# Kernel optimization log

Measured on AMD Instinct MI355X. Metric: run time of the kernel, lower is better.

Reference implementation:

```python
import jax, jax.numpy as jnp
from jax import lax
import numpy as np

B, H, W, C = 4, 64, 64, 128
L = H * W
DI = 2 * C   # mamba d_inner (expand=2)
NS = 16      # d_state
R = C // 16  # dt_rank
K = 4        # d_conv
S = 4        # scan branches: fwd, bwd, extra1, extra2


def setup_inputs():
    key = jax.random.key(0)
    ks = jax.random.split(key, 20)
    g = lambda i, shape, s=0.02: jax.random.normal(ks[i], shape, jnp.float32) * s
    return {
        "I1": jax.random.normal(ks[0], (B, L, C), jnp.float32),
        "fusion_resi": jax.random.normal(ks[1], (B, L, C), jnp.float32),
        "I2": jax.random.normal(ks[2], (B, L, C), jnp.float32),
        "fusion": jax.random.normal(ks[3], (B, L, C), jnp.float32),
        "ln1_w": jnp.ones((C,)), "ln1_b": jnp.zeros((C,)),
        "ln2_w": jnp.ones((C,)), "ln2_b": jnp.zeros((C,)),
        "ln3_w": jnp.ones((C,)), "ln3_b": jnp.zeros((C,)),
        "sp_w": g(4, (1, 2, 5, 5), 0.1),
        "ca_w1": g(5, (C // 4, C), 0.05),
        "ca_w2": g(6, (C, C // 4), 0.05),
        "dw_w": g(7, (C, 1, 3, 3), 0.1),
        "dw_b": jnp.zeros((C,)),
        "in_proj_w": g(8, (2 * DI, C)),
        "in_proj1_w": g(9, (DI, C)),
        "in_proj2_w": g(10, (DI, C)),
        "conv_w": g(11, (S, DI, K), 0.1),
        "conv_b": jnp.zeros((S, DI)),
        "xproj_w": g(12, (S, R + 2 * NS, DI)),
        "dt_w": g(13, (S, DI, R), 0.1),
        "dt_b": jnp.full((S, DI), -4.6, jnp.float32),  # softplus -> dt ~ 0.01
        "A_log": jnp.broadcast_to(jnp.log(jnp.arange(1, NS + 1, dtype=jnp.float32)), (S, DI, NS)) * 1.0,
        "Dskip": jnp.ones((S, DI)),
        "out_w": g(14, (C, DI)),
        "test_h": H, "test_w": W,
    }


def ln(x, w, b):
    mu = x.mean(-1, keepdims=True)
    xc = x - mu
    v = (xc * xc).mean(-1, keepdims=True)
    return xc / jnp.sqrt(v + 1e-5) * w + b


def sp_att(x, w, h, wd):
    # x: (B, N, C) -> (B, N, 1) spatial attention map
    Bb = x.shape[0]
    m = jnp.concatenate([x.mean(2, keepdims=True), x.max(2, keepdims=True)], 2)
    m = m.transpose(0, 2, 1).reshape(Bb, 2, h, wd)
    o = lax.conv_general_dilated(m, w, (1, 1), [(2, 2), (2, 2)],
                                 dimension_numbers=("NCHW", "OIHW", "NCHW"))
    return jax.nn.sigmoid(o).reshape(Bb, 1, -1).transpose(0, 2, 1)


def mamba_m3(xf, e1, e2, in_proj_w, in_proj1_w, in_proj2_w, conv_w, conv_b,
             xproj_w, dt_w, dt_b, A_log, Dskip, out_w):
    Bb, Ll, _ = xf.shape
    xz = xf @ in_proj_w.T                       # (B,L,2DI)
    x, z = xz[..., :DI], xz[..., DI:]
    # 4 branches: forward, backward (flipped), extra_emb1, extra_emb2
    u = jnp.stack([x, x[:, ::-1], e1 @ in_proj1_w.T, e2 @ in_proj2_w.T], 0)  # (S,B,L,DI)

    def causal_dwconv(xb, w, b):                # xb (B,L,DI)
        xp = jnp.pad(xb.transpose(0, 2, 1), ((0, 0), (0, 0), (K - 1, 0)))
        o = lax.conv_general_dilated(xp, w[:, None, :], (1,), "VALID",
                                     feature_group_count=DI,
                                     dimension_numbers=("NCH", "OIH", "NCH"))
        return (o + b[None, :, None]).transpose(0, 2, 1)

    uc = jax.nn.silu(jax.vmap(causal_dwconv)(u, conv_w, conv_b))        # (S,B,L,DI)
    proj = jnp.einsum("sbld,spd->sblp", uc, xproj_w)
    dt = jax.nn.softplus(jnp.einsum("sblr,sdr->sbld", proj[..., :R], dt_w)
                         + dt_b[:, None, None, :])                      # (S,B,L,DI)
    Bm, Cm = proj[..., R:R + NS], proj[..., R + NS:]                    # (S,B,L,NS)
    A = -jnp.exp(A_log)                                                 # (S,DI,NS)

    def step(h, inp):
        dt_t, B_t, C_t, u_t = inp                                       # (S,B,DI),(S,B,NS),(S,B,NS),(S,B,DI)
        dA = jnp.exp(dt_t[..., None] * A[:, None])                      # (S,B,DI,NS)
        h = h * dA + (dt_t * u_t)[..., None] * B_t[:, :, None, :]
        return h, jnp.einsum("sbdn,sbn->sbd", h, C_t)

    xs = tuple(t.transpose(2, 0, 1, 3) for t in (dt, Bm, Cm, uc))
    h0 = jnp.zeros((S, Bb, DI, NS), xf.dtype)
    _, ys = lax.scan(step, h0, xs)                                      # (L,S,B,DI)
    y = ys.transpose(1, 2, 0, 3) + uc * Dskip[:, None, None, :]         # (S,B,L,DI)
    y_tot = y[0] + y[1][:, ::-1] + y[2] + y[3]
    return (y_tot * jax.nn.silu(z)) @ out_w.T


def reference(I1, fusion_resi, I2, fusion, ln1_w, ln1_b, ln2_w, ln2_b, ln3_w,
              ln3_b, sp_w, ca_w1, ca_w2, dw_w, dw_b, in_proj_w, in_proj1_w,
              in_proj2_w, conv_w, conv_b, xproj_w, dt_w, dt_b, A_log, Dskip,
              out_w, test_h, test_w):
    fusion_resi = fusion + fusion_resi
    fusion = ln(fusion_resi, ln1_w, ln1_b)
    I2 = ln(I2 * sp_att(I2, sp_w, test_h, test_w), ln2_w, ln2_b)
    I1 = ln(I1 * sp_att(I1, sp_w, test_h, test_w), ln3_w, ln3_b)
    # note: original applies norm1/norm2/norm3 a second time here (faithful)
    gf = mamba_m3(ln(fusion, ln1_w, ln1_b), ln(I2, ln2_w, ln2_b),
                  ln(I1, ln3_w, ln3_b), in_proj_w, in_proj1_w, in_proj2_w,
                  conv_w, conv_b, xproj_w, dt_w, dt_b, A_log, Dskip, out_w)
    Bb, _, Cc = gf.shape
    f4 = gf.transpose(0, 2, 1).reshape(Bb, Cc, test_h, test_w)
    # ChannelAttention1 (already returns x*sig) then extra *fusion per source
    fc = lambda v: jnp.maximum(v @ ca_w1.T, 0.0) @ ca_w2.T
    sig = jax.nn.sigmoid(fc(f4.mean((2, 3))) + fc(f4.max((2, 3))))[:, :, None, None]
    f4 = (f4 * sig) * f4
    dw = lax.conv_general_dilated(f4, dw_w, (1, 1), [(1, 1), (1, 1)],
                                  feature_group_count=Cc,
                                  dimension_numbers=("NCHW", "OIHW", "NCHW"))
    dw = dw + dw_b[None, :, None, None]
    out = (dw + f4).reshape(Bb, Cc, -1).transpose(0, 2, 1)
    return out, fusion_resi
```

## Files before the change

kernel.cpp:

```cpp
#include <hip/hip_runtime.h>

#define DEVI __device__ __forceinline__

static constexpr int BB=4, CC=128, LLn=4096, DI=256, NS=16, RR=8, SS=4;
static constexpr int PP = RR + 2*NS;
static constexpr int CT = 64, NCH = LLn/CT;
static constexpr size_t BLC  = (size_t)BB*LLn*CC;
static constexpr size_t BLD  = (size_t)BB*LLn*DI;
static constexpr size_t SBLD = (size_t)SS*BLD;
static constexpr size_t SBLP = (size_t)SS*BB*LLn*PP;

static constexpr int OW_LN1W=0, OW_LN1B=128, OW_LN2W=256, OW_LN2B=384, OW_LN3W=512, OW_LN3B=640,
 OW_SPW=768, OW_CAW1=820, OW_CAW2=4916, OW_DWW=9012, OW_DWB=10164, OW_IPW=10292,
 OW_IP1W=75828, OW_IP2W=108596, OW_CVW=141364, OW_CVB=145460, OW_XPW=146484,
 OW_DTW=187444, OW_DTB=195636, OW_ALOG=196660, OW_DSK=213044, OW_OUTW=214068;
static constexpr int NW_RAW = 246836;
static constexpr int NW_END = 246848;

__constant__ int c_woff[22] = {OW_LN1W,OW_LN1B,OW_LN2W,OW_LN2B,OW_LN3W,OW_LN3B,OW_SPW,OW_CAW1,
 OW_CAW2,OW_DWW,OW_DWB,OW_IPW,OW_IP1W,OW_IP2W,OW_CVW,OW_CVB,OW_XPW,OW_DTW,OW_DTB,OW_ALOG,
 OW_DSK,OW_OUTW};
__constant__ int c_wsz[22]  = {128,128,128,128,128,128,50,4096,4096,1152,128,65536,32768,32768,
 4096,1024,40960,8192,1024,16384,1024,32768};

static constexpr size_t O_XF   = NW_END;
static constexpr size_t O_E1   = O_XF + BLC;
static constexpr size_t O_E2   = O_E1 + BLC;
static constexpr size_t O_Z    = O_E2 + BLC;
static constexpr size_t O_U    = O_Z + BLD;
static constexpr size_t O_UC   = O_U + SBLD;
static constexpr size_t O_PROJ = O_UC + SBLD;
static constexpr size_t O_SDT  = O_PROJ + SBLP;
static constexpr size_t O_H    = O_SDT + (size_t)SS*BB*NCH*DI;
static constexpr size_t O_M    = O_H + (size_t)SS*BB*NCH*DI*NS;
static constexpr size_t O_S    = O_M + 2*(size_t)BB*2*LLn;
static constexpr size_t O_GF   = O_S + 2*(size_t)BB*LLn;
static constexpr size_t O_PART = O_GF + BLC;
static constexpr size_t O_SIG  = O_PART + 2*(size_t)BB*32*CC;
static constexpr size_t WS_END = O_SIG + (size_t)BB*CC;

typedef __attribute__((ext_vector_type(8))) short short8v;
typedef __attribute__((ext_vector_type(4))) float f32x4;

DEVI float bfu2f(unsigned short s){ union{unsigned u; float f;} c; c.u = ((unsigned)s)<<16; return c.f; }
DEVI unsigned short f2bfu(float f){ union{float f; unsigned u;} c; c.f=f;
  unsigned r = c.u + 0x7FFFu + ((c.u>>16)&1u); return (unsigned short)(r>>16); }
DEVI bool bfmode(const void* ln1w){ return *(const unsigned*)ln1w == 0x3F803F80u; }
DEVI float2 ldin2(const void* p, int i, bool isbf){
  if(isbf){ unsigned v = *(const unsigned*)((const unsigned short*)p + i);
    return make_float2(bfu2f((unsigned short)(v & 0xFFFFu)), bfu2f((unsigned short)(v >> 16))); }
  const float* f = (const float*)p + i; return make_float2(f[0], f[1]);
}
DEVI float wsum(float v){
#pragma unroll
  for(int o=32;o;o>>=1) v += __shfl_xor(v,o,64);
  return v; }
DEVI float wmaxr(float v){
#pragma unroll
  for(int o=32;o;o>>=1) v = fmaxf(v, __shfl_xor(v,o,64));
  return v; }
DEVI float sigf(float x){ return 1.f/(1.f+__expf(-x)); }
DEVI float2 ln_wave(float2 x, const float* Wf, int ow, int ob, int lane){
  float mu = wsum(x.x + x.y) * (1.f/(float)CC);
  float dx = x.x - mu, dy = x.y - mu;
  float var = wsum(dx*dx + dy*dy) * (1.f/(float)CC);
  float rs = rsqrtf(var + 1e-5f);
  int c = 2*lane;
  return make_float2(dx*rs*Wf[ow+c] + Wf[ob+c], dy*rs*Wf[ow+c+1] + Wf[ob+c+1]);
}

struct Srcs { const void* p[22]; };

__global__ void k_wcvt(Srcs s, float* __restrict__ ws,
                       unsigned short* __restrict__ wip, unsigned short* __restrict__ wob){
  bool isbf = bfmode(s.p[0]);
  int idx = blockIdx.x*256 + threadIdx.x;
  if(idx >= NW_RAW) return;
  int t = 0;
  while(t < 21 && idx >= c_woff[t+1]) t++;
  int j = idx - c_woff[t];
  if(j >= c_wsz[t]) return;
  float v = isbf ? bfu2f(((const unsigned short*)s.p[t])[j]) : ((const float*)s.p[t])[j];
  ws[idx] = v;
  if(t==11)      wip[j]         = f2bfu(v);
  else if(t==12) wip[65536+j]   = f2bfu(v);
  else if(t==13) wip[98304+j]   = f2bfu(v);
  else if(t==21) wob[j]         = f2bfu(v);
}

__global__ void k_fuse(const void* fus, const void* fres, const void* ln1raw,
                       float* __restrict__ ws, float* __restrict__ outf,
                       unsigned short* __restrict__ xbf){
  bool isbf = bfmode(ln1raw);
  int lane = threadIdx.x & 63, wv = threadIdx.x >> 6;
  int row = blockIdx.x*4 + wv;
  int base = row*CC;
  float2 a = ldin2(fus, base+2*lane, isbf);
  float2 b = ldin2(fres, base+2*lane, isbf);
  float2 fr = make_float2(a.x+b.x, a.y+b.y);
  *(float2*)(outf + BLC + base + 2*lane) = fr;
  float2 y = ln_wave(fr, ws, OW_LN1W, OW_LN1B, lane);
  y = ln_wave(y, ws, OW_LN1W, OW_LN1B, lane);
  unsigned pk = (unsigned)f2bfu(y.x) | ((unsigned)f2bfu(y.y)<<16);
  *(unsigned*)&xbf[base + 2*lane] = pk;
}

__global__ void k_meanmax(const void* I1, const void* I2, const void* ln1raw, float* __restrict__ ws){
  bool isbf = bfmode(ln1raw);
  int lane = threadIdx.x & 63, wv = threadIdx.x >> 6;
  int g = blockIdx.x*4 + wv;
  int ten = g & 1, row = g >> 1;
  const void* src = ten ? I2 : I1;
  float2 x = ldin2(src, row*CC + 2*lane, isbf);
  float sm = wsum(x.x + x.y) * (1.f/(float)CC);
  float mx = wmaxr(fmaxf(x.x, x.y));
  if(lane == 0){
    int b = row >> 12, l = row & 4095;
    float* mt = ws + O_M + (size_t)ten*(BB*2*LLn);
    mt[(size_t)b*2*LLn + l] = sm;
    mt[(size_t)b*2*LLn + LLn + l] = mx;
  }
}

__global__ void k_spconv(float* __restrict__ ws){
  int idx = blockIdx.x*256 + threadIdx.x;
  int ten = idx >> 14, b = (idx>>12)&3, l = idx & 4095;
  int h = l >> 6, w = l & 63;
  const float* mt = ws + O_M + (size_t)ten*(BB*2*LLn) + (size_t)b*2*LLn;
  float acc = 0.f;
  for(int ci=0; ci<2; ci++)
    for(int kh=0; kh<5; kh++){
      int hh = h + kh - 2; if((unsigned)hh >= 64u) continue;
      for(int kw=0; kw<5; kw++){
        int wn = w + kw - 2; if((unsigned)wn >= 64u) continue;
        acc += mt[(size_t)ci*LLn + hh*64 + wn] * ws[OW_SPW + ci*25 + kh*5 + kw];
      }
    }
  ws[O_S + (size_t)ten*(BB*LLn) + (size_t)b*LLn + l] = sigf(acc);
}

__global__ void k_escale(const void* I1, const void* I2, const void* ln1raw,
                         float* __restrict__ ws, unsigned short* __restrict__ xbf){
  bool isbf = bfmode(ln1raw);
  int lane = threadIdx.x & 63, wv = threadIdx.x >> 6;
  int g = blockIdx.x*4 + wv;
  int ten = g & 1, row = g >> 1;
  const void* src = ten ? I1 : I2;
  float sc = ws[O_S + (ten ? 0 : (size_t)BB*LLn) + row];
  float2 x = ldin2(src, row*CC + 2*lane, isbf);
  x.x *= sc; x.y *= sc;
  int ow = ten ? OW_LN3W : OW_LN2W, ob = ten ? OW_LN3B : OW_LN2B;
  float2 y = ln_wave(x, ws, ow, ob, lane);
  y = ln_wave(y, ws, ow, ob, lane);
  unsigned short* eb = xbf + (ten ? 2*BLC : BLC);
  unsigned pk = (unsigned)f2bfu(y.x) | ((unsigned)f2bfu(y.y)<<16);
  *(unsigned*)&eb[row*CC + 2*lane] = pk;
}

__global__ __launch_bounds__(256) void k_gemm_bf(const unsigned short* __restrict__ Abf,
    const unsigned short* __restrict__ Wbf, float* __restrict__ out,
    int Kd, int N, int mode, float* __restrict__ u, float* __restrict__ z){
  __shared__ unsigned short As[64*64];
  __shared__ unsigned short Bs[64*64];
  const int tid = threadIdx.x, lane = tid & 63, w = tid >> 6;
  const int n0 = blockIdx.x*64, m0 = blockIdx.y*64;
  const int g = lane >> 4, rlo = lane & 15;
  f32x4 acc[4];
#pragma unroll
  for(int i=0;i<4;i++) acc[i] = (f32x4){0.f,0.f,0.f,0.f};
  const int nk = Kd >> 6;
  for(int kt=0; kt<nk; kt++){
#pragma unroll
    for(int it=0; it<2; it++){
      int idx = it*256 + tid, r = idx>>3, c = idx&7;
      uint4 av = *(const uint4*)&Abf[(size_t)(m0+r)*Kd + kt*64 + c*8];
      uint4 bv = *(const uint4*)&Wbf[(size_t)(n0+r)*Kd + kt*64 + c*8];
      int sw = (c*16) ^ ((r&7)<<4);
      *(uint4*)((char*)As + r*128 + sw) = av;
      *(uint4*)((char*)Bs + r*128 + sw) = bv;
    }
    __syncthreads();
#pragma unroll
    for(int ks=0; ks<2; ks++){
      int kb = ks*64 + g*16;
      int brow = w*16 + rlo;
      short8v bf = *(short8v*)((char*)Bs + brow*128 + (kb ^ ((rlo&7)<<4)));
#pragma unroll
      for(int rt=0; rt<4; rt++){
        int arow = rt*16 + rlo;
        short8v af = *(short8v*)((char*)As + arow*128 + (kb ^ ((rlo&7)<<4)));
        acc[rt] = __builtin_amdgcn_mfma_f32_16x16x32_bf16(af, bf, acc[rt], 0, 0, 0);
      }
    }
    __syncthreads();
  }
#pragma unroll
  for(int rt=0; rt<4; rt++){
#pragma unroll
    for(int j=0; j<4; j++){
      int m = m0 + rt*16 + g*4 + j;
      int n = n0 + w*16 + rlo;
      float val = acc[rt][j];
      if(mode == 0){
        out[(size_t)m*N + n] = val;
      } else {
        int b = m >> 12, l = m & (LLn-1);
        if(n < DI){
          u[((size_t)b*LLn + l)*DI + n] = val;
        } else {
          z[((size_t)b*LLn + l)*DI + (n-DI)] = val;
        }
      }
    }
  }
}

__global__ __launch_bounds__(256) void k_cxp(float* __restrict__ ws){
  __shared__ float ucl[16][260];
  __shared__ float wl[PP][260];
  int blk = blockIdx.x;
  int r0g = blk*16;
  int sb = r0g >> 12, s = sb >> 2, b = sb & 3;
  int l0 = r0g & 4095;
  int d = threadIdx.x;
  float4 cw = *(const float4*)&ws[OW_CVW + ((size_t)s*DI + d)*4];
  float cb = ws[OW_CVB + s*DI + d];
  const bool rev = (s == 1);
  const float* ub = ws + O_U + (rev ? ((size_t)b*LLn)*DI : ((size_t)sb*LLn)*DI);
  float w0, w1, w2;
  {
    int lm;
    lm = l0-3; w0 = (lm<0)?0.f:ub[(size_t)(rev?(LLn-1-lm):lm)*DI + d];
    lm = l0-2; w1 = (lm<0)?0.f:ub[(size_t)(rev?(LLn-1-lm):lm)*DI + d];
    lm = l0-1; w2 = (lm<0)?0.f:ub[(size_t)(rev?(LLn-1-lm):lm)*DI + d];
  }
#pragma unroll
  for(int r=0;r<16;r++){
    int l = l0 + r;
    float w3 = ub[(size_t)(rev?(LLn-1-l):l)*DI + d];
    float a = cb + cw.x*w0 + cw.y*w1 + cw.z*w2 + cw.w*w3;
    a *= sigf(a);
    ucl[r][d] = a;
    ws[O_UC + ((size_t)sb*LLn + l)*DI + d] = a;
    w0 = w1; w1 = w2; w2 = w3;
  }
#pragma unroll
  for(int i=0;i<10;i++){
    int e4 = i*256 + threadIdx.x; int r = e4>>6, c4 = e4&63;
    *(float4*)&wl[r][c4*4] = *(const float4*)&ws[OW_XPW + ((size_t)s*PP + r)*DI + c4*4];
  }
  __syncthreads();
  int r = threadIdx.x & 15, ps = threadIdx.x >> 4;
  for(int pp=0; pp<3; pp++){
    int p = ps + pp*16;
    if(p < PP){
      float4 acc = make_float4(0,0,0,0);
#pragma unroll 8
      for(int c4=0;c4<64;c4++){
        float4 a = *(const float4*)&ucl[r][c4*4];
        float4 bq = *(const float4*)&wl[p][c4*4];
        acc.x += a.x*bq.x; acc.y += a.y*bq.y; acc.z += a.z*bq.z; acc.w += a.w*bq.w;
      }
      ws[O_PROJ + (size_t)(r0g+r)*PP + p] = acc.x+acc.y+acc.z+acc.w;
    }
  }
}

template<bool PH3>
__global__ __launch_bounds__(256) void k_scan(float* __restrict__ ws){
  __shared__ float pl[CT*PP];
  int ch = blockIdx.x & (NCH-1), sb = blockIdx.x >> 6, s = sb >> 2;
  int d = threadIdx.x;
  size_t prow = ((size_t)sb*LLn + (size_t)ch*CT)*PP;
#pragma unroll
  for(int i=0;i<10;i++){ int idx = i*256 + threadIdx.x; pl[idx] = ws[O_PROJ + prow + idx]; }
  __syncthreads();
  float4 dtw0 = *(const float4*)&ws[OW_DTW + ((size_t)s*DI + d)*RR];
  float4 dtw1 = *(const float4*)&ws[OW_DTW + ((size_t)s*DI + d)*RR + 4];
  float dtb = ws[OW_DTB + s*DI + d];
  float an2[NS]; bool fast = true;
#pragma unroll
  for(int n=0;n<NS;n++){
    float a = -__expf(ws[OW_ALOG + ((size_t)s*DI + d)*NS + n]);
    an2[n] = a * 1.44269504f;
    fast = fast && (fabsf(a + (float)(n+1)) < 1e-4f);
  }
  float4 h0,h1,h2,h3;
  size_t hb = (((size_t)sb*NCH + ch)*DI + d)*NS;
  float* H = ws + O_H;
  if(PH3){
    h0 = *(const float4*)&H[hb];    h1 = *(const float4*)&H[hb+4];
    h2 = *(const float4*)&H[hb+8];  h3 = *(const float4*)&H[hb+12];
  } else {
    h0=h1=h2=h3=make_float4(0.f,0.f,0.f,0.f);
  }
  float dsk = PH3 ? ws[OW_DSK + s*DI + d] : 0.f;
  float sdt = 0.f;
  size_t ub = ((size_t)sb*LLn + (size_t)ch*CT)*DI + d;
  if(fast){
    for(int ll=0; ll<CT; ll++){
      const float* pr = &pl[ll*PP];
      float4 p0 = *(const float4*)pr, p1 = *(const float4*)(pr+4);
      float x = dtb + p0.x*dtw0.x + p0.y*dtw0.y + p0.z*dtw0.z + p0.w*dtw0.w
                    + p1.x*dtw1.x + p1.y*dtw1.y + p1.z*dtw1.z + p1.w*dtw1.w;
      float dt = (x > 15.f) ? x : __logf(1.f + __expf(x));
      float ut = ws[O_UC + ub + (size_t)ll*DI];
      float du = dt*ut;
      float e = __expf(-dt);
      float e2 = e*e, e4 = e2*e2;
      float4 da = make_float4(e, e2, e2*e, e4);
      float4 B0 = *(const float4*)(pr+8),  B1 = *(const float4*)(pr+12),
             B2 = *(const float4*)(pr+16), B3 = *(const float4*)(pr+20);
      if(PH3){
        float4 C0 = *(const float4*)(pr+24), C1 = *(const float4*)(pr+28),
               C2 = *(const float4*)(pr+32), C3 = *(const float4*)(pr+36);
        float y;
        h0.x = fmaf(h0.x, da.x, du*B0.x); y  = h0.x*C0.x;
        h0.y = fmaf(h0.y, da.y, du*B0.y); y = fmaf(h0.y, C0.y, y);
        h0.z = fmaf(h0.z, da.z, du*B0.z); y = fmaf(h0.z, C0.z, y);
        h0.w = fmaf(h0.w, da.w, du*B0.w); y = fmaf(h0.w, C0.w, y);
        da.x *= e4; da.y *= e4; da.z *= e4; da.w *= e4;
        h1.x = fmaf(h1.x, da.x, du*B1.x); y = fmaf(h1.x, C1.x, y);
        h1.y = fmaf(h1.y, da.y, du*B1.y); y = fmaf(h1.y, C1.y, y);
        h1.z = fmaf(h1.z, da.z, du*B1.z); y = fmaf(h1.z, C1.z, y);
        h1.w = fmaf(h1.w, da.w, du*B1.w); y = fmaf(h1.w, C1.w, y);
        da.x *= e4; da.y *= e4; da.z *= e4; da.w *= e4;
        h2.x = fmaf(h2.x, da.x, du*B2.x); y = fmaf(h2.x, C2.x, y);
        h2.y = fmaf(h2.y, da.y, du*B2.y); y = fmaf(h2.y, C2.y, y);
        h2.z = fmaf(h2.z, da.z, du*B2.z); y = fmaf(h2.z, C2.z, y);
        h2.w = fmaf(h2.w, da.w, du*B2.w); y = fmaf(h2.w, C2.w, y);
        da.x *= e4; da.y *= e4; da.z *= e4; da.w *= e4;
        h3.x = fmaf(h3.x, da.x, du*B3.x); y = fmaf(h3.x, C3.x, y);
        h3.y = fmaf(h3.y, da.y, du*B3.y); y = fmaf(h3.y, C3.y, y);
        h3.z = fmaf(h3.z, da.z, du*B3.z); y = fmaf(h3.z, C3.z, y);
        h3.w = fmaf(h3.w, da.w, du*B3.w); y = fmaf(h3.w, C3.w, y);
        ws[O_U + ub + (size_t)ll*DI] = y + ut*dsk;
      } else {
        h0.x = fmaf(h0.x, da.x, du*B0.x); h0.y = fmaf(h0.y, da.y, du*B0.y);
        h0.z = fmaf(h0.z, da.z, du*B0.z); h0.w = fmaf(h0.w, da.w, du*B0.w);
        da.x *= e4; da.y *= e4; da.z *= e4; da.w *= e4;
        h1.x = fmaf(h1.x, da.x, du*B1.x); h1.y = fmaf(h1.y, da.y, du*B1.y);
        h1.z = fmaf(h1.z, da.z, du*B1.z); h1.w = fmaf(h1.w, da.w, du*B1.w);
        da.x *= e4; da.y *= e4; da.z *= e4; da.w *= e4;
        h2.x = fmaf(h2.x, da.x, du*B2.x); h2.y = fmaf(h2.y, da.y, du*B2.y);
        h2.z = fmaf(h2.z, da.z, du*B2.z); h2.w = fmaf(h2.w, da.w, du*B2.w);
        da.x *= e4; da.y *= e4; da.z *= e4; da.w *= e4;
        h3.x = fmaf(h3.x, da.x, du*B3.x); h3.y = fmaf(h3.y, da.y, du*B3.y);
        h3.z = fmaf(h3.z, da.z, du*B3.z); h3.w = fmaf(h3.w, da.w, du*B3.w);
        sdt += dt;
      }
    }
  } else {
    float h[NS];
    h[0]=h0.x;h[1]=h0.y;h[2]=h0.z;h[3]=h0.w; h[4]=h1.x;h[5]=h1.y;h[6]=h1.z;h[7]=h1.w;
    h[8]=h2.x;h[9]=h2.y;h[10]=h2.z;h[11]=h2.w; h[12]=h3.x;h[13]=h3.y;h[14]=h3.z;h[15]=h3.w;
    for(int ll=0; ll<CT; ll++){
      const float* pr = &pl[ll*PP];
      float x = dtb;
      x += pr[0]*dtw0.x + pr[1]*dtw0.y + pr[2]*dtw0.z + pr[3]*dtw0.w;
      x += pr[4]*dtw1.x + pr[5]*dtw1.y + pr[6]*dtw1.z + pr[7]*dtw1.w;
      float dt = (x > 15.f) ? x : __logf(1.f + __expf(x));
      float ut = ws[O_UC + ub + (size_t)ll*DI];
      float du = dt*ut;
      if(PH3){
        float y = 0.f;
#pragma unroll
        for(int n=0;n<NS;n++){ float da = exp2f(an2[n]*dt); h[n] = h[n]*da + du*pr[RR+n]; y += h[n]*pr[RR+NS+n]; }
        ws[O_U + ub + (size_t)ll*DI] = y + ut*dsk;
      } else {
#pragma unroll
        for(int n=0;n<NS;n++){ float da = exp2f(an2[n]*dt); h[n] = h[n]*da + du*pr[RR+n]; }
        sdt += dt;
      }
    }
    h0=make_float4(h[0],h[1],h[2],h[3]); h1=make_float4(h[4],h[5],h[6],h[7]);
    h2=make_float4(h[8],h[9],h[10],h[11]); h3=make_float4(h[12],h[13],h[14],h[15]);
  }
  if(!PH3){
    *(float4*)&H[hb]    = h0; *(float4*)&H[hb+4]  = h1;
    *(float4*)&H[hb+8]  = h2; *(float4*)&H[hb+12] = h3;
    ws[O_SDT + ((size_t)sb*NCH + ch)*DI + d] = sdt;
  }
}

__global__ void k_scan2(float* __restrict__ ws){
  int t = blockIdx.x*256 + threadIdx.x;
  int n = t & (NS-1), d = (t>>4) & (DI-1), sb = t >> 12, s = sb >> 2;
  float an2 = -__expf(ws[OW_ALOG + ((size_t)s*DI + d)*NS + n]) * 1.44269504f;
  float hin = 0.f;
  float* H = ws + O_H;
  for(int c=0;c<NCH;c++){
    size_t hi = (((size_t)sb*NCH + c)*DI + d)*NS + n;
    float he = H[hi];
    float sd = ws[O_SDT + ((size_t)sb*NCH + c)*DI + d];
    H[hi] = hin;
    hin = he + exp2f(an2*sd)*hin;
  }
}

__global__ void k_gate(float* __restrict__ ws, unsigned short* __restrict__ gbf){
  int t = blockIdx.x*256 + threadIdx.x;
  int d4 = t & 63, l = (t>>6)&4095, b = t>>18;
  int d0 = d4*4;
  const float* y = ws + O_U;
  size_t i0 = ((size_t)(0*BB+b)*LLn + l)*DI + d0;
  size_t i1 = ((size_t)(1*BB+b)*LLn + (LLn-1-l))*DI + d0;
  size_t i2 = ((size_t)(2*BB+b)*LLn + l)*DI + d0;
  size_t i3 = ((size_t)(3*BB+b)*LLn + l)*DI + d0;
  float4 a = *(const float4*)&y[i0], bb4 = *(const float4*)&y[i1];
  float4 c = *(const float4*)&y[i2], dd = *(const float4*)&y[i3];
  size_t zi = ((size_t)b*LLn + l)*DI + d0;
  float4 zv = *(const float4*)&ws[O_Z + zi];
  float4 g;
  g.x = (a.x+bb4.x+c.x+dd.x) * (zv.x*sigf(zv.x));
  g.y = (a.y+bb4.y+c.y+dd.y) * (zv.y*sigf(zv.y));
  g.z = (a.z+bb4.z+c.z+dd.z) * (zv.z*sigf(zv.z));
  g.w = (a.w+bb4.w+c.w+dd.w) * (zv.w*sigf(zv.w));
  uint2 pk;
  pk.x = (unsigned)f2bfu(g.x) | ((unsigned)f2bfu(g.y)<<16);
  pk.y = (unsigned)f2bfu(g.z) | ((unsigned)f2bfu(g.w)<<16);
  *(uint2*)&gbf[zi] = pk;
}

__global__ void k_redmm(float* __restrict__ ws){
  int b = blockIdx.x >> 5, seg = blockIdx.x & 31, c = threadIdx.x;
  const float* gf = ws + O_GF;
  float sm = 0.f, mx = -3e38f;
  size_t base = ((size_t)b*LLn + (size_t)seg*128)*CC + c;
  for(int i=0;i<128;i++){ float v = gf[base + (size_t)i*CC]; sm += v; mx = fmaxf(mx, v); }
  ws[O_PART + ((size_t)b*32 + seg)*CC + c] = sm;
  ws[O_PART + (size_t)BB*32*CC + ((size_t)b*32 + seg)*CC + c] = mx;
}

__global__ void k_catt(float* __restrict__ ws){
  __shared__ float vm[CC], vx[CC], hm[32], hx[32];
  int b = blockIdx.x, c = threadIdx.x;
  float sm = 0.f, mx = -3e38f;
  for(int seg=0;seg<32;seg++){
    sm += ws[O_PART + ((size_t)b*32+seg)*CC + c];
    mx = fmaxf(mx, ws[O_PART + (size_t)BB*32*CC + ((size_t)b*32+seg)*CC + c]);
  }
  vm[c] = sm * (1.f/(float)LLn); vx[c] = mx;
  __syncthreads();
  if(c < 32){
    float am = 0.f, ax = 0.f;
    for(int k=0;k<CC;k++){ float w1 = ws[OW_CAW1 + c*CC + k]; am += vm[k]*w1; ax += vx[k]*w1; }
    hm[c] = fmaxf(am, 0.f); hx[c] = fmaxf(ax, 0.f);
  }
  __syncthreads();
  float om = 0.f, ox = 0.f;
  for(int k=0;k<32;k++){ float w2 = ws[OW_CAW2 + c*32 + k]; om += hm[k]*w2; ox += hx[k]*w2; }
  ws[O_SIG + (size_t)b*CC + c] = sigf(om + ox);
}

__global__ void k_final(float* __restrict__ ws, float* __restrict__ outf){
  int t = blockIdx.x*256 + threadIdx.x;
  int c4 = t & 31, l = (t>>5)&4095, b = t>>17;
  int h = l>>6, w = l&63;
  const float* gf = ws + O_GF;
  float4 sg = *(const float4*)&ws[O_SIG + (size_t)b*CC + c4*4];
  size_t rb = ((size_t)b*LLn)*CC;
  float4 gc = *(const float4*)&gf[rb + (size_t)l*CC + c4*4];
  float4 fc = make_float4(gc.x*gc.x*sg.x, gc.y*gc.y*sg.y, gc.z*gc.z*sg.z, gc.w*gc.w*sg.w);
  float4 acc = *(const float4*)&ws[OW_DWB + c4*4];
  float wv[4][9];
#pragma unroll
  for(int j=0;j<4;j++)
#pragma unroll
    for(int q=0;q<9;q++) wv[j][q] = ws[OW_DWW + (c4*4+j)*9 + q];
#pragma unroll
  for(int kh=0;kh<3;kh++){
    int hh = h + kh - 1; if((unsigned)hh >= 64u) continue;
#pragma unroll
    for(int kw=0;kw<3;kw++){
      int wn = w + kw - 1; if((unsigned)wn >= 64u) continue;
      float4 g = *(const float4*)&gf[rb + (size_t)(hh*64+wn)*CC + c4*4];
      int q = kh*3+kw;
      acc.x += wv[0][q]*g.x*g.x*sg.x;
      acc.y += wv[1][q]*g.y*g.y*sg.y;
      acc.z += wv[2][q]*g.z*g.z*sg.z;
      acc.w += wv[3][q]*g.w*g.w*sg.w;
    }
  }
  float4 o = make_float4(acc.x+fc.x, acc.y+fc.y, acc.z+fc.z, acc.w+fc.w);
  size_t ob = ((size_t)b*LLn + l)*CC + c4*4;
  *(float4*)&outf[ob] = o;
}

extern "C" void kernel_launch(void* const* d_in, const int* in_sizes, int n_in,
                              void* d_out, int out_size, void* d_ws, size_t ws_size,
                              hipStream_t stream){
  (void)in_sizes; (void)n_in; (void)out_size;
  if(ws_size < WS_END*sizeof(float)) return;
  float* ws = (float*)d_ws;
  float* outf = (float*)d_out;
  const void* I1 = d_in[0]; const void* FRES = d_in[1];
  const void* I2 = d_in[2]; const void* FUS  = d_in[3];
  const void* LN1RAW = d_in[4];

  unsigned short* xbf   = (unsigned short*)(ws + O_H);
  unsigned short* gbf   = xbf;
  unsigned short* wipbf = (unsigned short*)(ws + O_GF);
  unsigned short* wobf  = (unsigned short*)(ws + O_PART);

  Srcs sr;
  for(int i=0;i<22;i++) sr.p[i] = d_in[4+i];
  k_wcvt<<<(NW_RAW+255)/256, 256, 0, stream>>>(sr, ws, wipbf, wobf);
  k_fuse<<<4096, 256, 0, stream>>>(FUS, FRES, LN1RAW, ws, outf, xbf);
  k_meanmax<<<8192, 256, 0, stream>>>(I1, I2, LN1RAW, ws);
  k_spconv<<<128, 256, 0, stream>>>(ws);
  k_escale<<<8192, 256, 0, stream>>>(I1, I2, LN1RAW, ws, xbf);
  k_gemm_bf<<<dim3(8,256), 256, 0, stream>>>(xbf,         wipbf,       nullptr,        128, 512, 1, ws+O_U, ws+O_Z);
  k_gemm_bf<<<dim3(4,256), 256, 0, stream>>>(xbf+BLC,     wipbf+65536, ws+O_U+2*BLD,   128, 256, 0, nullptr, nullptr);
  k_gemm_bf<<<dim3(4,256), 256, 0, stream>>>(xbf+2*BLC,   wipbf+98304, ws+O_U+3*BLD,   128, 256, 0, nullptr, nullptr);
  k_cxp<<<4096, 256, 0, stream>>>(ws);
  k_scan<false><<<SS*BB*NCH, 256, 0, stream>>>(ws);
  k_scan2<<<256, 256, 0, stream>>>(ws);
  k_scan<true><<<SS*BB*NCH, 256, 0, stream>>>(ws);
  k_gate<<<4096, 256, 0, stream>>>(ws, gbf);
  k_gemm_bf<<<dim3(2,256), 256, 0, stream>>>(gbf, wobf, ws+O_GF, 256, 128, 0, nullptr, nullptr);
  k_redmm<<<128, 128, 0, stream>>>(ws);
  k_catt<<<4, 128, 0, stream>>>(ws);
  k_final<<<2048, 256, 0, stream>>>(ws, outf);
}
```

Baseline: 295.4 us.

## Split conv and x_proj, run x_proj on bf16 MFMA GEMM with padded weights

```diff
diff --git a/kernel.cpp b/kernel.cpp
--- a/kernel.cpp
+++ b/kernel.cpp
@@ -71,8 +71,14 @@
 
 struct Srcs { const void* p[22]; };
 
+__global__ void k_xwpad(unsigned* __restrict__ xw32){
+  int i = blockIdx.x*256 + threadIdx.x;
+  xw32[i] = 0u;
+}
+
 __global__ void k_wcvt(Srcs s, float* __restrict__ ws,
-                       unsigned short* __restrict__ wip, unsigned short* __restrict__ wob){
+                       unsigned short* __restrict__ wip, unsigned short* __restrict__ wob,
+                       unsigned short* __restrict__ xw){
   bool isbf = bfmode(s.p[0]);
   int idx = blockIdx.x*256 + threadIdx.x;
   if(idx >= NW_RAW) return;
@@ -86,6 +92,10 @@
   else if(t==12) wip[65536+j]   = f2bfu(v);
   else if(t==13) wip[98304+j]   = f2bfu(v);
   else if(t==21) wob[j]         = f2bfu(v);
+  else if(t==16){
+    int sid = j / 10240, rem = j % 10240;
+    xw[((size_t)sid*64 + rem/256)*256 + (rem%256)] = f2bfu(v);
+  }
 }
 
 __global__ void k_fuse(const void* fus, const void* fres, const void* ln1raw,
@@ -165,6 +175,7 @@
   const int tid = threadIdx.x, lane = tid & 63, w = tid >> 6;
   const int n0 = blockIdx.x*64, m0 = blockIdx.y*64;
   const int g = lane >> 4, rlo = lane & 15;
+  if(mode == 2) Wbf += (size_t)(m0 >> 14) * (64*256);
   f32x4 acc[4];
 #pragma unroll
   for(int i=0;i<4;i++) acc[i] = (f32x4){0.f,0.f,0.f,0.f};
@@ -201,8 +212,8 @@
       int m = m0 + rt*16 + g*4 + j;
       int n = n0 + w*16 + rlo;
       float val = acc[rt][j];
-      if(mode == 0){
-        out[(size_t)m*N + n] = val;
+      if(mode != 1){
+        if(n < N) out[(size_t)m*N + n] = val;
       } else {
         int b = m >> 12, l = m & (LLn-1);
         if(n < DI){
@@ -215,59 +226,35 @@
   }
 }
 
-__global__ __launch_bounds__(256) void k_cxp(float* __restrict__ ws){
-  __shared__ float ucl[16][260];
-  __shared__ float wl[PP][260];
-  int blk = blockIdx.x;
-  int r0g = blk*16;
-  int sb = r0g >> 12, s = sb >> 2, b = sb & 3;
-  int l0 = r0g & 4095;
-  int d = threadIdx.x;
-  float4 cw = *(const float4*)&ws[OW_CVW + ((size_t)s*DI + d)*4];
-  float cb = ws[OW_CVB + s*DI + d];
+__global__ void k_conv(float* __restrict__ ws, unsigned short* __restrict__ ucbf){
+  int t = blockIdx.x*256 + threadIdx.x;
+  int d4 = t & 63, l = (t>>6)&4095, sb = t>>18, s = sb>>2, b = sb&3;
+  int d0 = d4*4;
+  const float* wp = ws + OW_CVW + ((size_t)s*DI + d0)*4;
+  float wv[16];
+#pragma unroll
+  for(int q=0;q<16;q++) wv[q] = wp[q];
+  float4 acc = *(const float4*)&ws[OW_CVB + s*DI + d0];
   const bool rev = (s == 1);
   const float* ub = ws + O_U + (rev ? ((size_t)b*LLn)*DI : ((size_t)sb*LLn)*DI);
-  float w0, w1, w2;
-  {
-    int lm;
-    lm = l0-3; w0 = (lm<0)?0.f:ub[(size_t)(rev?(LLn-1-lm):lm)*DI + d];
-    lm = l0-2; w1 = (lm<0)?0.f:ub[(size_t)(rev?(LLn-1-lm):lm)*DI + d];
-    lm = l0-1; w2 = (lm<0)?0.f:ub[(size_t)(rev?(LLn-1-lm):lm)*DI + d];
-  }
-#pragma unroll
-  for(int r=0;r<16;r++){
-    int l = l0 + r;
-    float w3 = ub[(size_t)(rev?(LLn-1-l):l)*DI + d];
-    float a = cb + cw.x*w0 + cw.y*w1 + cw.z*w2 + cw.w*w3;
-    a *= sigf(a);
-    ucl[r][d] = a;
-    ws[O_UC + ((size_t)sb*LLn + l)*DI + d] = a;
-    w0 = w1; w1 = w2; w2 = w3;
-  }
-#pragma unroll
-  for(int i=0;i<10;i++){
-    int e4 = i*256 + threadIdx.x; int r = e4>>6, c4 = e4&63;
-    *(float4*)&wl[r][c4*4] = *(const float4*)&ws[OW_XPW + ((size_t)s*PP + r)*DI + c4*4];
-  }
-  __syncthreads();
-  int r = threadIdx.x & 15, ps = threadIdx.x >> 4;
-  for(int pp=0; pp<3; pp++){
-    int p = ps + pp*16;
-    if(p < PP){
-      float4 acc = make_float4(0,0,0,0);
-#pragma unroll 8
-      for(int c4=0;c4<64;c4++){
-        float4 a = *(const float4*)&ucl[r][c4*4];
-        float4 bq = *(const float4*)&wl[p][c4*4];
-        acc.x += a.x*bq.x; acc.y += a.y*bq.y; acc.z += a.z*bq.z; acc.w += a.w*bq.w;
-      }
-      ws[O_PROJ + (size_t)(r0g+r)*PP + p] = acc.x+acc.y+acc.z+acc.w;
-    }
-  }
+#pragma unroll
+  for(int k=0;k<4;k++){
+    int lk = l - 3 + k;
+    if(lk >= 0){
+      int li = rev ? (LLn-1-lk) : lk;
+      float4 uv = *(const float4*)&ub[(size_t)li*DI + d0];
+      acc.x += wv[0*4+k]*uv.x; acc.y += wv[1*4+k]*uv.y;
+      acc.z += wv[2*4+k]*uv.z; acc.w += wv[3*4+k]*uv.w;
+    }
+  }
+  acc.x *= sigf(acc.x); acc.y *= sigf(acc.y); acc.z *= sigf(acc.z); acc.w *= sigf(acc.w);
+  ushort4 o4; o4.x=f2bfu(acc.x); o4.y=f2bfu(acc.y); o4.z=f2bfu(acc.z); o4.w=f2bfu(acc.w);
+  *(ushort4*)&ucbf[((size_t)sb*LLn + l)*DI + d0] = o4;
 }
 
 template<bool PH3>
-__global__ __launch_bounds__(256) void k_scan(float* __restrict__ ws){
+__global__ __launch_bounds__(256) void k_scan(float* __restrict__ ws,
+                                              const unsigned short* __restrict__ ucbf){
   __shared__ float pl[CT*PP];
   int ch = blockIdx.x & (NCH-1), sb = blockIdx.x >> 6, s = sb >> 2;
   int d = threadIdx.x;
@@ -304,7 +291,7 @@
       float x = dtb + p0.x*dtw0.x + p0.y*dtw0.y + p0.z*dtw0.z + p0.w*dtw0.w
                     + p1.x*dtw1.x + p1.y*dtw1.y + p1.z*dtw1.z + p1.w*dtw1.w;
       float dt = (x > 15.f) ? x : __logf(1.f + __expf(x));
-      float ut = ws[O_UC + ub + (size_t)ll*DI];
+      float ut = bfu2f(ucbf[ub + (size_t)ll*DI]);
       float du = dt*ut;
       float e = __expf(-dt);
       float e2 = e*e, e4 = e2*e2;
@@ -360,7 +347,7 @@
       x += pr[0]*dtw0.x + pr[1]*dtw0.y + pr[2]*dtw0.z + pr[3]*dtw0.w;
       x += pr[4]*dtw1.x + pr[5]*dtw1.y + pr[6]*dtw1.z + pr[7]*dtw1.w;
       float dt = (x > 15.f) ? x : __logf(1.f + __expf(x));
-      float ut = ws[O_UC + ub + (size_t)ll*DI];
+      float ut = bfu2f(ucbf[ub + (size_t)ll*DI]);
       float du = dt*ut;
       if(PH3){
         float y = 0.f;
@@ -502,10 +489,13 @@
   unsigned short* gbf   = xbf;
   unsigned short* wipbf = (unsigned short*)(ws + O_GF);
   unsigned short* wobf  = (unsigned short*)(ws + O_PART);
+  unsigned short* xwbf  = (unsigned short*)(ws + O_XF);
+  unsigned short* ucbf  = (unsigned short*)(ws + O_UC);
 
   Srcs sr;
   for(int i=0;i<22;i++) sr.p[i] = d_in[4+i];
-  k_wcvt<<<(NW_RAW+255)/256, 256, 0, stream>>>(sr, ws, wipbf, wobf);
+  k_xwpad<<<128, 256, 0, stream>>>((unsigned*)xwbf);
+  k_wcvt<<<(NW_RAW+255)/256, 256, 0, stream>>>(sr, ws, wipbf, wobf, xwbf);
   k_fuse<<<4096, 256, 0, stream>>>(FUS, FRES, LN1RAW, ws, outf, xbf);
   k_meanmax<<<8192, 256, 0, stream>>>(I1, I2, LN1RAW, ws);
   k_spconv<<<128, 256, 0, stream>>>(ws);
@@ -513,10 +503,11 @@
   k_gemm_bf<<<dim3(8,256), 256, 0, stream>>>(xbf,         wipbf,       nullptr,        128, 512, 1, ws+O_U, ws+O_Z);
   k_gemm_bf<<<dim3(4,256), 256, 0, stream>>>(xbf+BLC,     wipbf+65536, ws+O_U+2*BLD,   128, 256, 0, nullptr, nullptr);
   k_gemm_bf<<<dim3(4,256), 256, 0, stream>>>(xbf+2*BLC,   wipbf+98304, ws+O_U+3*BLD,   128, 256, 0, nullptr, nullptr);
-  k_cxp<<<4096, 256, 0, stream>>>(ws);
-  k_scan<false><<<SS*BB*NCH, 256, 0, stream>>>(ws);
+  k_conv<<<16384, 256, 0, stream>>>(ws, ucbf);
+  k_gemm_bf<<<dim3(1,1024), 256, 0, stream>>>(ucbf, xwbf, ws+O_PROJ, 256, 40, 2, nullptr, nullptr);
+  k_scan<false><<<SS*BB*NCH, 256, 0, stream>>>(ws, ucbf);
   k_scan2<<<256, 256, 0, stream>>>(ws);
-  k_scan<true><<<SS*BB*NCH, 256, 0, stream>>>(ws);
+  k_scan<true><<<SS*BB*NCH, 256, 0, stream>>>(ws, ucbf);
   k_gate<<<4096, 256, 0, stream>>>(ws, gbf);
   k_gemm_bf<<<dim3(2,256), 256, 0, stream>>>(gbf, wobf, ws+O_GF, 256, 128, 0, nullptr, nullptr);
   k_redmm<<<128, 128, 0, stream>>>(ws);
```

Result: faster. 285.0 us (-3.5%).
